# Optimization experiments

Hardware: AMD Instinct MI355X
Metric: run time of the kernel (lower is better)

## Reference

```python
import jax, jax.numpy as jnp
import numpy as np

M = 2.0      # margin from __init__
EPS = 1e-6   # CosineSimilarity eps


def setup_inputs() -> dict:
    key = jax.random.key(0)
    k1, k2 = jax.random.split(key)
    ys = jax.random.normal(k1, (4096, 2048), dtype=jnp.float32)
    labels = jax.random.randint(k2, (4096,), 0, 10, dtype=jnp.int64)
    return {"ys": ys, "labels": labels}


def reference(ys, labels):
    b = ys.shape[0]
    # Normalized Gram matrix == pairwise cosine similarity (eps-clamped norms)
    norms = jnp.clip(jnp.linalg.norm(ys, axis=-1, keepdims=True), EPS)
    yn = ys / norms
    cos = yn @ yn.T                                   # [b, b]
    same = labels[:, None] == labels[None, :]         # d == 1 branch
    # same label -> clamp(m - cos, 0)^2 ; diff label -> cos^2
    pair_loss = jnp.where(same,
                          jnp.square(jax.nn.relu(M - cos)),
                          jnp.square(cos))
    # strict lower triangle i > j
    tril = jnp.tril(jnp.ones((b, b), dtype=bool), k=-1)
    n_pair = b * (b - 1) // 2
    return jnp.sum(jnp.where(tril, pair_loss, 0.0)) / n_pair
```

## Files before the change

kernel.cpp:

```cpp
#include <hip/hip_runtime.h>


#define ROWS 4096
#define KDIM 2048
#define NJOBS 1056
#define BK 128
#define FSCALE 32.0f
#define FSCALE2_INV (1.0f / (FSCALE * FSCALE))
#define SCALE_ONE 0x7F7F7F7F

typedef float f32x4 __attribute__((ext_vector_type(4)));
typedef int i32x4 __attribute__((ext_vector_type(4)));
typedef int i32x8 __attribute__((ext_vector_type(8)));

__device__ __forceinline__ void async_copy16(const unsigned char* g, unsigned char* l) {
    __builtin_amdgcn_global_load_lds(
        (const __attribute__((address_space(1))) void*)g,
        (__attribute__((address_space(3))) void*)l,
        16, 0, 0);
}

__global__ __launch_bounds__(256) void normalize_rows(
    const float* __restrict__ ys, unsigned int* __restrict__ yn) {
    int row = blockIdx.x;
    const float4* src = (const float4*)(ys + (size_t)row * KDIM);
    float4 vals[2];
    float ss = 0.f;
#pragma unroll
    for (int i = 0; i < 2; ++i) {
        float4 v = src[threadIdx.x + i * 256];
        vals[i] = v;
        ss += v.x * v.x + v.y * v.y + v.z * v.z + v.w * v.w;
    }
#pragma unroll
    for (int off = 32; off > 0; off >>= 1) ss += __shfl_down(ss, off);
    __shared__ float red[4];
    int lane = threadIdx.x & 63, wv = threadIdx.x >> 6;
    if (lane == 0) red[wv] = ss;
    __syncthreads();
    float tot = red[0] + red[1] + red[2] + red[3];
    float inv = FSCALE / fmaxf(sqrtf(tot), 1e-6f);
    unsigned int* dst = yn + (size_t)row * (KDIM / 4);
#pragma unroll
    for (int i = 0; i < 2; ++i) {
        float4 v = vals[i];
        int p = __builtin_amdgcn_cvt_pk_fp8_f32(v.x * inv, v.y * inv, 0, false);
        p = __builtin_amdgcn_cvt_pk_fp8_f32(v.z * inv, v.w * inv, p, true);
        dst[threadIdx.x + i * 256] = (unsigned int)p;
    }
}

__global__ __launch_bounds__(256) void gram_loss(
    const unsigned char* __restrict__ yn, const int* __restrict__ labels,
    float* __restrict__ partials) {
    int t = (blockIdx.x & 7) * (NJOBS / 8) + (blockIdx.x >> 3);
    int bi = (int)((sqrtf((float)(4 * t + 1)) - 1.0f) * 0.5f);
    while (bi * (bi + 1) > t) --bi;
    while ((bi + 1) * (bi + 2) <= t) ++bi;
    int bj = t - bi * (bi + 1);

    __shared__ __attribute__((aligned(16))) unsigned char As[128 * BK];
    __shared__ __attribute__((aligned(16))) unsigned char Bs[64 * BK];
    __shared__ int labI[128];
    __shared__ int labJ[64];
    __shared__ float red[4];

    int tid = threadIdx.x, lane = tid & 63, wv = tid >> 6;
    int wr = wv >> 1, wc = wv & 1;
    int rowA = bi * 128, rowB = bj * 64;

    if (tid < 128) labI[tid] = labels[rowA + tid];
    else if (tid < 192) labJ[tid - 128] = labels[rowB + tid - 128];

    int srow = lane >> 3;
    int sbyte = ((lane & 7) ^ srow) * 16;

    f32x4 zero = {0.f, 0.f, 0.f, 0.f};
    f32x4 acc[4][2];
#pragma unroll
    for (int m = 0; m < 4; ++m)
#pragma unroll
        for (int n = 0; n < 2; ++n) acc[m][n] = zero;

    int colB = lane & 15;
    int kq = lane >> 4;

    for (int k0 = 0; k0 < KDIM; k0 += BK) {
        __syncthreads();
#pragma unroll
        for (int it = 0; it < 6; ++it) {
            int chunk = it * 4 + wv;
            if (chunk < 16) {
                int rr = chunk * 8 + srow;
                async_copy16(yn + (size_t)(rowA + rr) * KDIM + k0 + sbyte,
                             As + chunk * 1024);
            } else {
                int c2 = chunk - 16;
                int rr = c2 * 8 + srow;
                async_copy16(yn + (size_t)(rowB + rr) * KDIM + k0 + sbyte,
                             Bs + c2 * 1024);
            }
        }
        __syncthreads();

        i32x8 af8[4];
#pragma unroll
        for (int m = 0; m < 4; ++m) {
            int row = wr * 64 + m * 16 + colB;
            int byte0 = (row * BK + kq * 32) ^ ((row & 7) << 4);
            i32x4 lo = *(const i32x4*)(As + byte0);
            i32x4 hi = *(const i32x4*)(As + (byte0 ^ 16));
            af8[m] = (i32x8){lo.x, lo.y, lo.z, lo.w, hi.x, hi.y, hi.z, hi.w};
        }
        i32x8 bf8v[2];
#pragma unroll
        for (int n = 0; n < 2; ++n) {
            int row = wc * 32 + n * 16 + colB;
            int byte0 = (row * BK + kq * 32) ^ ((row & 7) << 4);
            i32x4 lo = *(const i32x4*)(Bs + byte0);
            i32x4 hi = *(const i32x4*)(Bs + (byte0 ^ 16));
            bf8v[n] = (i32x8){lo.x, lo.y, lo.z, lo.w, hi.x, hi.y, hi.z, hi.w};
        }
#pragma unroll
        for (int m = 0; m < 4; ++m)
#pragma unroll
            for (int n = 0; n < 2; ++n)
                acc[m][n] = __builtin_amdgcn_mfma_scale_f32_16x16x128_f8f6f4(
                    af8[m], bf8v[n], acc[m][n],
                    0, 0,
                    0, SCALE_ONE,
                    0, SCALE_ONE);
    }

    float lsum = 0.f;
#pragma unroll
    for (int m = 0; m < 4; ++m) {
#pragma unroll
        for (int n = 0; n < 2; ++n) {
#pragma unroll
            for (int j = 0; j < 4; ++j) {
                int ti = wr * 64 + m * 16 + kq * 4 + j;
                int tj = wc * 32 + n * 16 + colB;
                int gi = rowA + ti, gj = rowB + tj;
                if (gi > gj) {
                    float c = acc[m][n][j] * FSCALE2_INV;
                    float v = (labI[ti] == labJ[tj]) ? fmaxf(2.0f - c, 0.0f) : c;
                    lsum += v * v;
                }
            }
        }
    }
#pragma unroll
    for (int off = 32; off > 0; off >>= 1) lsum += __shfl_down(lsum, off);
    if (lane == 0) red[wv] = lsum;
    __syncthreads();
    if (tid == 0) partials[blockIdx.x] = red[0] + red[1] + red[2] + red[3];
}

__global__ __launch_bounds__(256) void finalize(
    const float* __restrict__ partials, float* __restrict__ out) {
    float s = 0.f;
    for (int i = threadIdx.x; i < NJOBS; i += 256) s += partials[i];
#pragma unroll
    for (int off = 32; off > 0; off >>= 1) s += __shfl_down(s, off);
    __shared__ float red[4];
    int lane = threadIdx.x & 63, wv = threadIdx.x >> 6;
    if (lane == 0) red[wv] = s;
    __syncthreads();
    if (threadIdx.x == 0) {
        const double npair = (double)ROWS * (ROWS - 1) / 2.0;
        out[0] = (float)((double)(red[0] + red[1] + red[2] + red[3]) / npair);
    }
}

extern "C" void kernel_launch(void* const* d_in, const int* in_sizes, int n_in,
                              void* d_out, int out_size, void* d_ws, size_t ws_size,
                              hipStream_t stream) {
    const float* ys = (const float*)d_in[0];
    const int* labels = (const int*)d_in[1];
    float* out = (float*)d_out;

    unsigned char* yn = (unsigned char*)d_ws;
    float* partials = (float*)((char*)d_ws + (size_t)ROWS * KDIM);

    normalize_rows<<<ROWS, 256, 0, stream>>>(ys, (unsigned int*)yn);
    gram_loss<<<NJOBS, 256, 0, stream>>>(yn, labels, partials);
    finalize<<<1, 256, 0, stream>>>(partials, out);
}
```

Before: 46.74 us.

## Repack fp8 rows into MFMA fragment layout and load operands directly from global

Adds a repack kernel that rearranges the normalized fp8 matrix into 16-row groups laid out in MFMA fragment order, so each lane's 32-byte operand is contiguous. The gram kernel then drops the LDS staging and the per-step barriers, reading A and B fragments straight from global memory (through L2/L1) inside an unrolled loop. This is meant to remove the synchronisation and LDS round trips. The costs are an extra kernel launch, an extra 8MB write and read, and global-memory latency sitting directly in the MFMA loop. Operands are also re-fetched redundantly across waves that share rows.

Result: slower. 57.41 us (+22.8%).

```diff
diff --git a/kernel.cpp b/kernel.cpp
--- a/kernel.cpp
+++ b/kernel.cpp
@@ -4,21 +4,15 @@
 #define ROWS 4096
 #define KDIM 2048
 #define NJOBS 1056
-#define BK 128
+#define NSTEPS 16
 #define FSCALE 32.0f
 #define FSCALE2_INV (1.0f / (FSCALE * FSCALE))
 #define SCALE_ONE 0x7F7F7F7F
+#define GRPSZ 32768
 
 typedef float f32x4 __attribute__((ext_vector_type(4)));
 typedef int i32x4 __attribute__((ext_vector_type(4)));
 typedef int i32x8 __attribute__((ext_vector_type(8)));
-
-__device__ __forceinline__ void async_copy16(const unsigned char* g, unsigned char* l) {
-    __builtin_amdgcn_global_load_lds(
-        (const __attribute__((address_space(1))) void*)g,
-        (__attribute__((address_space(3))) void*)l,
-        16, 0, 0);
-}
 
 __global__ __launch_bounds__(256) void normalize_rows(
     const float* __restrict__ ys, unsigned int* __restrict__ yn) {
@@ -50,8 +44,23 @@
     }
 }
 
+__global__ __launch_bounds__(256) void repack(
+    const unsigned char* __restrict__ yn, unsigned char* __restrict__ pk) {
+    int g = blockIdx.x;
+    int tid = threadIdx.x, lane = tid & 63, w = tid >> 6;
+    int row = lane >> 2, off = (lane & 3) * 8;
+    const unsigned char* src = yn + (size_t)(g * 16 + row) * KDIM + off;
+    unsigned char* dst = pk + (size_t)g * GRPSZ + row * 32 + off;
+#pragma unroll
+    for (int i = 0; i < 16; ++i) {
+        int kb = i * 4 + w;
+        *(unsigned long long*)(dst + kb * 512) =
+            *(const unsigned long long*)(src + kb * 32);
+    }
+}
+
 __global__ __launch_bounds__(256) void gram_loss(
-    const unsigned char* __restrict__ yn, const int* __restrict__ labels,
+    const unsigned char* __restrict__ pk, const int* __restrict__ labels,
     float* __restrict__ partials) {
     int t = (blockIdx.x & 7) * (NJOBS / 8) + (blockIdx.x >> 3);
     int bi = (int)((sqrtf((float)(4 * t + 1)) - 1.0f) * 0.5f);
@@ -59,8 +68,6 @@
     while ((bi + 1) * (bi + 2) <= t) ++bi;
     int bj = t - bi * (bi + 1);
 
-    __shared__ __attribute__((aligned(16))) unsigned char As[128 * BK];
-    __shared__ __attribute__((aligned(16))) unsigned char Bs[64 * BK];
     __shared__ int labI[128];
     __shared__ int labJ[64];
     __shared__ float red[4];
@@ -72,8 +79,12 @@
     if (tid < 128) labI[tid] = labels[rowA + tid];
     else if (tid < 192) labJ[tid - 128] = labels[rowB + tid - 128];
 
-    int srow = lane >> 3;
-    int sbyte = ((lane & 7) ^ srow) * 16;
+    int colB = lane & 15;
+    int kq = lane >> 4;
+
+    size_t laneoff = (size_t)kq * 512 + colB * 32;
+    const unsigned char* baseA = pk + (size_t)(bi * 8 + wr * 4) * GRPSZ + laneoff;
+    const unsigned char* baseB = pk + (size_t)(bj * 4 + wc * 2) * GRPSZ + laneoff;
 
     f32x4 zero = {0.f, 0.f, 0.f, 0.f};
     f32x4 acc[4][2];
@@ -82,55 +93,34 @@
 #pragma unroll
         for (int n = 0; n < 2; ++n) acc[m][n] = zero;
 
-    int colB = lane & 15;
-    int kq = lane >> 4;
-
-    for (int k0 = 0; k0 < KDIM; k0 += BK) {
-        __syncthreads();
-#pragma unroll
-        for (int it = 0; it < 6; ++it) {
-            int chunk = it * 4 + wv;
-            if (chunk < 16) {
-                int rr = chunk * 8 + srow;
-                async_copy16(yn + (size_t)(rowA + rr) * KDIM + k0 + sbyte,
-                             As + chunk * 1024);
-            } else {
-                int c2 = chunk - 16;
-                int rr = c2 * 8 + srow;
-                async_copy16(yn + (size_t)(rowB + rr) * KDIM + k0 + sbyte,
-                             Bs + c2 * 1024);
-            }
-        }
-        __syncthreads();
-
+#pragma unroll 2
+    for (int ts = 0; ts < NSTEPS; ++ts) {
+        size_t ko = (size_t)ts * 2048;
         i32x8 af8[4];
 #pragma unroll
         for (int m = 0; m < 4; ++m) {
-            int row = wr * 64 + m * 16 + colB;
-            int byte0 = (row * BK + kq * 32) ^ ((row & 7) << 4);
-            i32x4 lo = *(const i32x4*)(As + byte0);
-            i32x4 hi = *(const i32x4*)(As + (byte0 ^ 16));
+            const unsigned char* p = baseA + (size_t)m * GRPSZ + ko;
+            i32x4 lo = *(const i32x4*)p;
+            i32x4 hi = *(const i32x4*)(p + 16);
             af8[m] = (i32x8){lo.x, lo.y, lo.z, lo.w, hi.x, hi.y, hi.z, hi.w};
         }
-        i32x8 bf8v[2];
 #pragma unroll
         for (int n = 0; n < 2; ++n) {
-            int row = wc * 32 + n * 16 + colB;
-            int byte0 = (row * BK + kq * 32) ^ ((row & 7) << 4);
-            i32x4 lo = *(const i32x4*)(Bs + byte0);
-            i32x4 hi = *(const i32x4*)(Bs + (byte0 ^ 16));
-            bf8v[n] = (i32x8){lo.x, lo.y, lo.z, lo.w, hi.x, hi.y, hi.z, hi.w};
-        }
+            const unsigned char* p = baseB + (size_t)n * GRPSZ + ko;
+            i32x4 lo = *(const i32x4*)p;
+            i32x4 hi = *(const i32x4*)(p + 16);
+            i32x8 bn = (i32x8){lo.x, lo.y, lo.z, lo.w, hi.x, hi.y, hi.z, hi.w};
 #pragma unroll
-        for (int m = 0; m < 4; ++m)
-#pragma unroll
-            for (int n = 0; n < 2; ++n)
+            for (int m = 0; m < 4; ++m)
                 acc[m][n] = __builtin_amdgcn_mfma_scale_f32_16x16x128_f8f6f4(
-                    af8[m], bf8v[n], acc[m][n],
+                    af8[m], bn, acc[m][n],
                     0, 0,
                     0, SCALE_ONE,
                     0, SCALE_ONE);
+        }
     }
+
+    __syncthreads();
 
     float lsum = 0.f;
 #pragma unroll
@@ -181,9 +171,11 @@
     float* out = (float*)d_out;
 
     unsigned char* yn = (unsigned char*)d_ws;
-    float* partials = (float*)((char*)d_ws + (size_t)ROWS * KDIM);
+    unsigned char* pkb = (unsigned char*)d_ws + (size_t)ROWS * KDIM;
+    float* partials = (float*)((char*)d_ws + 2 * (size_t)ROWS * KDIM);
 
     normalize_rows<<<ROWS, 256, 0, stream>>>(ys, (unsigned int*)yn);
-    gram_loss<<<NJOBS, 256, 0, stream>>>(yn, labels, partials);
+    repack<<<ROWS / 16, 256, 0, stream>>>(yn, pkb);
+    gram_loss<<<NJOBS, 256, 0, stream>>>(pkb, labels, partials);
     finalize<<<1, 256, 0, stream>>>(partials, out);
 }
```
